# Performance work log

Hardware: AMD Instinct MI355X
Metric: run time of the kernel (lower is better)

Reference implementation:

```python
import jax, jax.numpy as jnp
import numpy as np
from jax import lax

# Faithful JAX translation of Laplacian_Forward_Model.forward(acc=False).
# The opaque approximate multiplier (mul_wrapper) is modeled as an exact
# multiply, under which approx_sharp and accurate_sharp produce identical
# values; the original assigns x.data = approx result (values) while grads
# flow through the accurate path, so with exact multiply the single accurate
# path (with straight-through floor) reproduces the full forward math.

LAPLACIAN = np.array([-1.0, -1.0, -1.0, -1.0, 8.0, -1.0, -1.0, -1.0, -1.0]) / 8.0


def setup_inputs() -> dict:
    key = jax.random.key(0)
    k_in, = jax.random.split(key, 1)
    B = 16384
    n_mult = 1  # len(mul_approx_func_arr)
    inp = jax.random.uniform(k_in, (B, 1, 32, 32), dtype=jnp.float32) * 255.0
    weight = jnp.asarray(np.tile(LAPLACIAN, (n_mult, 1)), dtype=jnp.float32)          # (n_mult, 9)
    weight_factor = jnp.asarray(np.tile(np.array([8.0]), (n_mult, 1)), dtype=jnp.float32)  # (n_mult, 1)
    return {"input": inp, "weight": weight, "weight_factor": weight_factor}


def _sharp(x, ker):
    # depthwise 3x3 conv, padding 1 (C=1 so plain conv)
    B = x.shape[0]
    conv = lax.conv_general_dilated(x, ker, window_strides=(1, 1),
                                    padding=((1, 1), (1, 1)),
                                    dimension_numbers=("NCHW", "OIHW", "NCHW"))
    flat = conv.reshape(B, -1)
    cmax = lax.stop_gradient(flat.max(axis=1)).reshape(B, 1, 1, 1)
    cmin = lax.stop_gradient(flat.min(axis=1)).reshape(B, 1, 1, 1)
    mod = (conv - cmin) / jnp.maximum(cmax - cmin, 1e-6) * 255.0
    sharpened = x + mod
    sflat = sharpened.reshape(B, -1)
    smax = lax.stop_gradient(sflat.max(axis=1)).reshape(B, 1, 1, 1)
    smin = lax.stop_gradient(sflat.min(axis=1)).reshape(B, 1, 1, 1)
    res = jnp.clip((sharpened - smin) / jnp.clip(smax - smin, 1e-6, 255.0) * 255.0, 0.0, 255.0)
    # result.data = floor(result.data): straight-through floor
    return res + lax.stop_gradient(jnp.floor(res) - res)


def reference(input, weight, weight_factor):
    n_mult = weight.shape[0]
    outs = []
    for ii in range(n_mult):  # small fixed loop over approx-multiplier variants
        wc = jnp.clip(weight[ii], -0.999, 0.999)            # clamp + hardtanh(-1,1)
        wf = jnp.clip(weight_factor[ii], 1.001, 254.999)    # clamp + hardtanh(1,255)
        ker = (wc * wf).reshape(1, 1, 3, 3).astype(input.dtype)
        outs.append(_sharp(input, ker))
    return jnp.stack(outs, 0)  # (n_mult, B, 1, 32, 32)
```

## Files before the change

### kernel.cpp

```cpp
#include <hip/hip_runtime.h>
#include <math.h>


#define S 40

template <int CTRL>
__device__ __forceinline__ float dppmov(float x) {
    return __int_as_float(__builtin_amdgcn_update_dpp(
        __float_as_int(x), __float_as_int(x), CTRL, 0xf, 0xf, false));
}

__device__ __forceinline__ void wave64_minmax(float& mn, float& mx) {
    mn = fminf(mn, dppmov<0x111>(mn)); mx = fmaxf(mx, dppmov<0x111>(mx));
    mn = fminf(mn, dppmov<0x112>(mn)); mx = fmaxf(mx, dppmov<0x112>(mx));
    mn = fminf(mn, dppmov<0x114>(mn)); mx = fmaxf(mx, dppmov<0x114>(mx));
    mn = fminf(mn, dppmov<0x118>(mn)); mx = fmaxf(mx, dppmov<0x118>(mx));
    mn = fminf(mn, dppmov<0x142>(mn)); mx = fmaxf(mx, dppmov<0x142>(mx));
    mn = fminf(mn, dppmov<0x143>(mn)); mx = fmaxf(mx, dppmov<0x143>(mx));
}

__global__ __launch_bounds__(64) void laplacian_fwd_kernel(
    const float* __restrict__ in,
    const float* __restrict__ weight,
    const float* __restrict__ wfac,
    float* __restrict__ out)
{
    __shared__ float img[34 * S];

    const int b = blockIdx.x;
    const int t = threadIdx.x;
    const float* src = in + (size_t)b * 1024;
    float* dst = out + (size_t)b * 1024;

    const int rbase = t >> 3;
    const int col0  = (t & 7) << 2;

    float4 x4[4];
#pragma unroll
    for (int i = 0; i < 4; ++i)
        x4[i] = *(const float4*)(src + i * 256 + t * 4);

    if (t < 40) { img[t] = 0.0f; img[33 * S + t] = 0.0f; }
    if (t < 32) { img[(t + 1) * S + 3] = 0.0f; img[(t + 1) * S + 36] = 0.0f; }

    const float wf = fminf(fmaxf(wfac[0], 1.001f), 254.999f);
    float k[9];
#pragma unroll
    for (int i = 0; i < 9; ++i)
        k[i] = fminf(fmaxf(weight[i], -0.999f), 0.999f) * wf;

#pragma unroll
    for (int i = 0; i < 4; ++i)
        *(float4*)&img[(i * 8 + rbase + 1) * S + (col0 + 4)] = x4[i];
    __syncthreads();

    float conv[4][4];
#pragma unroll
    for (int i = 0; i < 4; ++i) {
        const int row = i * 8 + rbase;
        const float* pt = &img[ row      * S + col0];
        const float* pm = &img[(row + 1) * S + col0];
        const float* pb = &img[(row + 2) * S + col0];
        const float  tl = pt[3], tr = pt[8];
        const float4 tm = *(const float4*)(pt + 4);
        const float  ml = pm[3], mr = pm[8];
        const float  bl = pb[3], br = pb[8];
        const float4 bm = *(const float4*)(pb + 4);
        const float4 m  = x4[i];
        conv[i][0] = k[0]*tl   + k[1]*tm.x + k[2]*tm.y
                   + k[3]*ml   + k[4]*m.x  + k[5]*m.y
                   + k[6]*bl   + k[7]*bm.x + k[8]*bm.y;
        conv[i][1] = k[0]*tm.x + k[1]*tm.y + k[2]*tm.z
                   + k[3]*m.x  + k[4]*m.y  + k[5]*m.z
                   + k[6]*bm.x + k[7]*bm.y + k[8]*bm.z;
        conv[i][2] = k[0]*tm.y + k[1]*tm.z + k[2]*tm.w
                   + k[3]*m.y  + k[4]*m.z  + k[5]*m.w
                   + k[6]*bm.y + k[7]*bm.z + k[8]*bm.w;
        conv[i][3] = k[0]*tm.z + k[1]*tm.w + k[2]*tr
                   + k[3]*m.z  + k[4]*m.w  + k[5]*mr
                   + k[6]*bm.z + k[7]*bm.w + k[8]*br;
    }

    float mn = conv[0][0], mx = conv[0][0];
#pragma unroll
    for (int i = 0; i < 4; ++i)
#pragma unroll
        for (int j = 0; j < 4; ++j) {
            mn = fminf(mn, conv[i][j]);
            mx = fmaxf(mx, conv[i][j]);
        }
    wave64_minmax(mn, mx);
    const float cmin = __builtin_amdgcn_readlane(__float_as_int(mn), 63) == 0
                       ? __int_as_float(__builtin_amdgcn_readlane(__float_as_int(mn), 63))
                       : __int_as_float(__builtin_amdgcn_readlane(__float_as_int(mn), 63));
    const float cmax = __int_as_float(__builtin_amdgcn_readlane(__float_as_int(mx), 63));

    const float inv1 = 255.0f / fmaxf(cmax - cmin, 1e-6f);
    float sh[4][4];
#pragma unroll
    for (int i = 0; i < 4; ++i) {
        sh[i][0] = x4[i].x + (conv[i][0] - cmin) * inv1;
        sh[i][1] = x4[i].y + (conv[i][1] - cmin) * inv1;
        sh[i][2] = x4[i].z + (conv[i][2] - cmin) * inv1;
        sh[i][3] = x4[i].w + (conv[i][3] - cmin) * inv1;
    }

    mn = sh[0][0]; mx = sh[0][0];
#pragma unroll
    for (int i = 0; i < 4; ++i)
#pragma unroll
        for (int j = 0; j < 4; ++j) {
            mn = fminf(mn, sh[i][j]);
            mx = fmaxf(mx, sh[i][j]);
        }
    wave64_minmax(mn, mx);
    const float smin = __int_as_float(__builtin_amdgcn_readlane(__float_as_int(mn), 63));
    const float smax = __int_as_float(__builtin_amdgcn_readlane(__float_as_int(mx), 63));

    const float inv2 = 255.0f / fminf(fmaxf(smax - smin, 1e-6f), 255.0f);
#pragma unroll
    for (int i = 0; i < 4; ++i) {
        float4 o;
        o.x = floorf(fminf(fmaxf((sh[i][0] - smin) * inv2, 0.0f), 255.0f));
        o.y = floorf(fminf(fmaxf((sh[i][1] - smin) * inv2, 0.0f), 255.0f));
        o.z = floorf(fminf(fmaxf((sh[i][2] - smin) * inv2, 0.0f), 255.0f));
        o.w = floorf(fminf(fmaxf((sh[i][3] - smin) * inv2, 0.0f), 255.0f));
        *(float4*)(dst + i * 256 + t * 4) = o;
    }
}

extern "C" void kernel_launch(void* const* d_in, const int* in_sizes, int n_in,
                              void* d_out, int out_size, void* d_ws, size_t ws_size,
                              hipStream_t stream) {
    const float* in   = (const float*)d_in[0];
    const float* w    = (const float*)d_in[1];
    const float* wfac = (const float*)d_in[2];
    float* out = (float*)d_out;
    const int B = in_sizes[0] / 1024;
    laplacian_fwd_kernel<<<B, 64, 0, stream>>>(in, w, wfac, out);
}
```

Before: 112.0 us.

## Process two images per wave in 256-thread blocks with nontemporal stores

Each block now holds four waves, and each wave handles two images using its own shared-memory slice. Both images' loads are issued before any compute, so more global reads are in flight at once. Block-wide syncs become wave barriers, and the padded row stride shrinks to 36 by sharing each row's right pad with the next row's left pad. Output is written with nontemporal stores to bypass the cache. The cost is more registers and shared memory per block, and the two images in a wave are processed one after the other.

After: 111.7 us. About the same (-0.3%).

```diff
diff --git a/kernel.cpp b/kernel.cpp
--- a/kernel.cpp
+++ b/kernel.cpp
@@ -2,7 +2,10 @@
 #include <math.h>
 
 
-#define S 40
+#define S 36
+#define SLICE 1228
+
+typedef float floatx4 __attribute__((ext_vector_type(4)));
 
 template <int CTRL>
 __device__ __forceinline__ float dppmov(float x) {
@@ -19,48 +22,26 @@
     mn = fminf(mn, dppmov<0x143>(mn)); mx = fmaxf(mx, dppmov<0x143>(mx));
 }
 
-__global__ __launch_bounds__(64) void laplacian_fwd_kernel(
-    const float* __restrict__ in,
-    const float* __restrict__ weight,
-    const float* __restrict__ wfac,
-    float* __restrict__ out)
+__device__ __forceinline__ void process_image(
+    float* __restrict__ sm, const float4* x4, const float* k,
+    float* __restrict__ dst, int lane)
 {
-    __shared__ float img[34 * S];
+    const int rbase = lane >> 3;
+    const int col0  = (lane & 7) << 2;
 
-    const int b = blockIdx.x;
-    const int t = threadIdx.x;
-    const float* src = in + (size_t)b * 1024;
-    float* dst = out + (size_t)b * 1024;
-
-    const int rbase = t >> 3;
-    const int col0  = (t & 7) << 2;
-
-    float4 x4[4];
+    __builtin_amdgcn_wave_barrier();
 #pragma unroll
     for (int i = 0; i < 4; ++i)
-        x4[i] = *(const float4*)(src + i * 256 + t * 4);
-
-    if (t < 40) { img[t] = 0.0f; img[33 * S + t] = 0.0f; }
-    if (t < 32) { img[(t + 1) * S + 3] = 0.0f; img[(t + 1) * S + 36] = 0.0f; }
-
-    const float wf = fminf(fmaxf(wfac[0], 1.001f), 254.999f);
-    float k[9];
-#pragma unroll
-    for (int i = 0; i < 9; ++i)
-        k[i] = fminf(fmaxf(weight[i], -0.999f), 0.999f) * wf;
-
-#pragma unroll
-    for (int i = 0; i < 4; ++i)
-        *(float4*)&img[(i * 8 + rbase + 1) * S + (col0 + 4)] = x4[i];
-    __syncthreads();
+        *(float4*)&sm[(i * 8 + rbase + 1) * S + (col0 + 4)] = x4[i];
+    __builtin_amdgcn_wave_barrier();
 
     float conv[4][4];
 #pragma unroll
     for (int i = 0; i < 4; ++i) {
         const int row = i * 8 + rbase;
-        const float* pt = &img[ row      * S + col0];
-        const float* pm = &img[(row + 1) * S + col0];
-        const float* pb = &img[(row + 2) * S + col0];
+        const float* pt = &sm[ row      * S + col0];
+        const float* pm = &sm[(row + 1) * S + col0];
+        const float* pb = &sm[(row + 2) * S + col0];
         const float  tl = pt[3], tr = pt[8];
         const float4 tm = *(const float4*)(pt + 4);
         const float  ml = pm[3], mr = pm[8];
@@ -80,6 +61,7 @@
                    + k[3]*m.z  + k[4]*m.w  + k[5]*mr
                    + k[6]*bm.z + k[7]*bm.w + k[8]*br;
     }
+    __builtin_amdgcn_wave_barrier();
 
     float mn = conv[0][0], mx = conv[0][0];
 #pragma unroll
@@ -90,9 +72,7 @@
             mx = fmaxf(mx, conv[i][j]);
         }
     wave64_minmax(mn, mx);
-    const float cmin = __builtin_amdgcn_readlane(__float_as_int(mn), 63) == 0
-                       ? __int_as_float(__builtin_amdgcn_readlane(__float_as_int(mn), 63))
-                       : __int_as_float(__builtin_amdgcn_readlane(__float_as_int(mn), 63));
+    const float cmin = __int_as_float(__builtin_amdgcn_readlane(__float_as_int(mn), 63));
     const float cmax = __int_as_float(__builtin_amdgcn_readlane(__float_as_int(mx), 63));
 
     const float inv1 = 255.0f / fmaxf(cmax - cmin, 1e-6f);
@@ -120,13 +100,54 @@
     const float inv2 = 255.0f / fminf(fmaxf(smax - smin, 1e-6f), 255.0f);
 #pragma unroll
     for (int i = 0; i < 4; ++i) {
-        float4 o;
+        floatx4 o;
         o.x = floorf(fminf(fmaxf((sh[i][0] - smin) * inv2, 0.0f), 255.0f));
         o.y = floorf(fminf(fmaxf((sh[i][1] - smin) * inv2, 0.0f), 255.0f));
         o.z = floorf(fminf(fmaxf((sh[i][2] - smin) * inv2, 0.0f), 255.0f));
         o.w = floorf(fminf(fmaxf((sh[i][3] - smin) * inv2, 0.0f), 255.0f));
-        *(float4*)(dst + i * 256 + t * 4) = o;
+        __builtin_nontemporal_store(o, (floatx4*)(dst + i * 256 + lane * 4));
     }
+}
+
+__global__ __launch_bounds__(256) void laplacian_fwd_kernel(
+    const float* __restrict__ in,
+    const float* __restrict__ weight,
+    const float* __restrict__ wfac,
+    float* __restrict__ out)
+{
+    __shared__ float lds[4 * SLICE];
+
+    const int t    = threadIdx.x;
+    const int w    = t >> 6;
+    const int lane = t & 63;
+    float* sm = &lds[w * SLICE];
+
+    const int W = blockIdx.x * 4 + w;
+    const size_t base0 = (size_t)(2 * W) * 1024;
+    const size_t base1 = base0 + 1024;
+
+    float4 xa[4];
+#pragma unroll
+    for (int i = 0; i < 4; ++i)
+        xa[i] = *(const float4*)(in + base0 + i * 256 + lane * 4);
+
+    if (lane < 36) { sm[lane] = 0.0f; sm[33 * S + lane] = 0.0f; }
+    if (lane < 32) { sm[(lane + 1) * S] = 0.0f; sm[(lane + 1) * S + 3] = 0.0f; }
+    if (lane == 0) sm[34 * S] = 0.0f;
+
+    const float wf = fminf(fmaxf(wfac[0], 1.001f), 254.999f);
+    float k[9];
+#pragma unroll
+    for (int i = 0; i < 9; ++i)
+        k[i] = fminf(fmaxf(weight[i], -0.999f), 0.999f) * wf;
+
+    float4 xb[4];
+#pragma unroll
+    for (int i = 0; i < 4; ++i)
+        xb[i] = *(const float4*)(in + base1 + i * 256 + lane * 4);
+
+    process_image(sm, xa, k, out + base0, lane);
+    process_image(sm, xb, k, out + base1, lane);
 }
 
 extern "C" void kernel_launch(void* const* d_in, const int* in_sizes, int n_in,
@@ -137,5 +158,6 @@
     const float* wfac = (const float*)d_in[2];
     float* out = (float*)d_out;
     const int B = in_sizes[0] / 1024;
-    laplacian_fwd_kernel<<<B, 64, 0, stream>>>(in, w, wfac, out);
+    const int nblocks = B / 8;
+    laplacian_fwd_kernel<<<nblocks, 256, 0, stream>>>(in, w, wfac, out);
 }
```
